# Optimization experiments

Hardware: AMD Instinct MI355X
Metric: run time of the kernel (lower is better)

Reference implementation:

```python
import jax, jax.numpy as jnp
import numpy as np

N_NODES = 50000
N_EDGES = 800000
IN_CH = 128
HEADS = 4
HID = 32  # per-head dim; heads*hid = 128
N_GRAPHS = 128


def setup_inputs() -> dict:
    key = jax.random.key(0)
    ks = jax.random.split(key, 32)
    d = {}
    d["x"] = jax.random.normal(ks[0], (N_NODES, IN_CH), dtype=jnp.float32)
    d["edge_index"] = jax.random.randint(ks[1], (2, N_EDGES), 0, N_NODES, dtype=jnp.int64)
    d["batch"] = jnp.sort(jax.random.randint(ks[2], (N_NODES,), 0, N_GRAPHS, dtype=jnp.int64))
    HD = HEADS * HID
    names = [("wq1", (IN_CH, HD)), ("bq1", (HD,)), ("wk1", (IN_CH, HD)), ("bk1", (HD,)),
             ("wv1", (IN_CH, HD)), ("bv1", (HD,)), ("ws1", (IN_CH, HD)), ("bs1", (HD,)),
             ("wq2", (HD, HD)), ("bq2", (HD,)), ("wk2", (HD, HD)), ("bk2", (HD,)),
             ("wv2", (HD, HD)), ("bv2", (HD,)), ("ws2", (HD, HD)), ("bs2", (HD,)),
             ("wl", (HD, HD)), ("bl", (HD,)), ("wl2", (HD, 1)), ("bl2", (1,))]
    for i, (nm, shp) in enumerate(names):
        d[nm] = jax.random.normal(ks[3 + i], shp, dtype=jnp.float32) * 0.05
    return d


def _transformer_conv(x, src, dst, wq, bq, wk, bk, wv, bv, ws, bs):
    """PyG TransformerConv: multi-head dot-product attention over edges,
    softmax normalized per destination node, plus linear root/skip term."""
    N = x.shape[0]
    q = (x @ wq + bq).reshape(N, HEADS, HID)
    k = (x @ wk + bk).reshape(N, HEADS, HID)
    v = (x @ wv + bv).reshape(N, HEADS, HID)
    # edge scores: [E, H]
    e = jnp.einsum('ehd,ehd->eh', q[dst], k[src]) * np.float32(1.0 / np.sqrt(HID))
    # segment softmax over incoming edges of each destination node
    m = jax.ops.segment_max(e, dst, num_segments=N)
    a = jnp.exp(e - m[dst])
    s = jax.ops.segment_sum(a, dst, num_segments=N)
    alpha = a / s[dst]  # [E, H]
    msg = alpha[:, :, None] * v[src]  # [E, H, D]
    out = jax.ops.segment_sum(msg, dst, num_segments=N).reshape(N, HEADS * HID)
    return out + x @ ws + bs  # root weight (skip) term


def reference(x, edge_index, batch,
              wq1, bq1, wk1, bk1, wv1, bv1, ws1, bs1,
              wq2, bq2, wk2, bk2, wv2, bv2, ws2, bs2,
              wl, bl, wl2, bl2):
    src, dst = edge_index[0], edge_index[1]
    h = _transformer_conv(x, src, dst, wq1, bq1, wk1, bk1, wv1, bv1, ws1, bs1)
    h = jax.nn.relu(h)
    h = _transformer_conv(h, src, dst, wq2, bq2, wk2, bk2, wv2, bv2, ws2, bs2)
    h = jax.nn.relu(h)
    h = h @ wl + bl
    h = h @ wl2 + bl2  # [N, 1]
    # global mean pool over graphs
    sums = jax.ops.segment_sum(h, batch, num_segments=N_GRAPHS)
    cnts = jax.ops.segment_sum(jnp.ones((h.shape[0], 1), h.dtype), batch, num_segments=N_GRAPHS)
    return sums / jnp.maximum(cnts, 1.0)
```

## Files before the change

### kernel.cpp

```cpp
#include <hip/hip_runtime.h>
#include <hip/hip_bf16.h>
#include <math.h>

#define NNODES 50000
#define NEDGES 800000
#define NGRAPHS 128
#define SCAN_B ((NNODES + 255) / 256)

typedef __attribute__((ext_vector_type(8))) short bf16x8;
typedef __attribute__((ext_vector_type(4))) float f32x4;

__device__ __forceinline__ unsigned short f2bf(float f) {
    unsigned int u = __float_as_uint(f);
    return (unsigned short)((u + 0x7FFFu + ((u >> 16) & 1u)) >> 16);
}
__device__ __forceinline__ float2 bf2f2(unsigned int u) {
    float2 f;
    f.x = __uint_as_float(u << 16);
    f.y = __uint_as_float(u & 0xFFFF0000u);
    return f;
}

__global__ void count_edges(const int* __restrict__ ei, int* __restrict__ cnt) {
    int e = blockIdx.x * 256 + threadIdx.x;
    if (e < NEDGES) atomicAdd(&cnt[ei[NEDGES + e]], 1);
}

__global__ __launch_bounds__(256)
void scan_pass1(const int* __restrict__ cnt, int* __restrict__ bsum) {
    const int t = threadIdx.x;
    const int i = blockIdx.x * 256 + t;
    int v = (i < NNODES) ? cnt[i] : 0;
#pragma unroll
    for (int off = 32; off > 0; off >>= 1) v += __shfl_xor(v, off, 64);
    __shared__ int ws[4];
    if ((t & 63) == 0) ws[t >> 6] = v;
    __syncthreads();
    if (t == 0) bsum[blockIdx.x] = ws[0] + ws[1] + ws[2] + ws[3];
}

__global__ __launch_bounds__(256)
void scan_pass2(const int* __restrict__ bsum, int* __restrict__ boff) {
    const int t = threadIdx.x;
    const int v = (t < SCAN_B) ? bsum[t] : 0;
    __shared__ int a[256];
    a[t] = v;
    __syncthreads();
    for (int off = 1; off < 256; off <<= 1) {
        const int u = (t >= off) ? a[t - off] : 0;
        __syncthreads();
        a[t] += u;
        __syncthreads();
    }
    if (t < SCAN_B) boff[t] = a[t] - v;
}

__global__ __launch_bounds__(256)
void scan_pass3(const int* __restrict__ cnt, const int* __restrict__ boff,
                int* __restrict__ rowptr, int* __restrict__ wpos) {
    const int t = threadIdx.x;
    const int i = blockIdx.x * 256 + t;
    const int v = (i < NNODES) ? cnt[i] : 0;
    __shared__ int a[256];
    a[t] = v;
    __syncthreads();
    for (int off = 1; off < 256; off <<= 1) {
        const int u = (t >= off) ? a[t - off] : 0;
        __syncthreads();
        a[t] += u;
        __syncthreads();
    }
    if (i < NNODES) {
        const int e = boff[blockIdx.x] + a[t] - v;
        rowptr[i] = e;
        wpos[i]   = e;
    }
    if (i == 0) rowptr[NNODES] = NEDGES;
}

__global__ void fill_csr(const int* __restrict__ ei, int* __restrict__ wpos,
                         int* __restrict__ colsrc) {
    int e = blockIdx.x * 256 + threadIdx.x;
    if (e < NEDGES) {
        int d = ei[NEDGES + e];
        int slot = atomicAdd(&wpos[d], 1);
        colsrc[slot] = ei[e];
    }
}

__global__ void fuse_wl(const float* __restrict__ wl, const float* __restrict__ bl,
                        const float* __restrict__ wl2, const float* __restrict__ bl2,
                        float* __restrict__ wf, float* __restrict__ bf) {
    int t = threadIdx.x;
    float s = 0.f;
    for (int j = 0; j < 128; ++j) s += wl[t * 128 + j] * wl2[j];
    wf[t] = s;
    if (t == 0) {
        float s2 = 0.f;
        for (int j = 0; j < 128; ++j) s2 += bl[j] * wl2[j];
        bf[0] = s2 + bl2[0];
    }
}

__global__ void prep_w(const float* __restrict__ wq, const float* __restrict__ wk,
                       const float* __restrict__ wv, const float* __restrict__ wsk,
                       unsigned short* __restrict__ Wt) {
    const int sel = blockIdx.y;
    const float* W = sel == 0 ? wq : sel == 1 ? wk : sel == 2 ? wv : wsk;
    const int idx = blockIdx.x * 256 + threadIdx.x;
    const int col = idx & 127;
    const int k   = idx >> 7;
    Wt[sel * 16384 + col * 128 + k] = f2bf(W[k * 128 + col]);
}

__global__ __launch_bounds__(256)
void gemm_qkvs(const float* __restrict__ F, const unsigned short* __restrict__ Wt,
               const float* __restrict__ bq, const float* __restrict__ bk,
               const float* __restrict__ bv, const float* __restrict__ bsk,
               float* __restrict__ Q, unsigned short* __restrict__ Kb,
               float* __restrict__ V, float* __restrict__ H) {
    __shared__ __align__(16) unsigned short As[128][136];
    __shared__ __align__(16) unsigned short Bt[64][136];
    const int t    = threadIdx.x;
    const int m0   = blockIdx.x * 128;
    const int lane = t & 63;
    const int w    = t >> 6;
    const int l15  = lane & 15;
    const int lg   = lane >> 4;

    {
        const int row = t >> 1;
        const int kh  = (t & 1) * 64;
        const int gr  = min(m0 + row, NNODES - 1);
        const float* src = &F[(size_t)gr * 128 + kh];
#pragma unroll
        for (int p = 0; p < 16; ++p) {
            const float4 v = *(const float4*)&src[p * 4];
            ushort4 u;
            u.x = f2bf(v.x); u.y = f2bf(v.y); u.z = f2bf(v.z); u.w = f2bf(v.w);
            *(ushort4*)&As[row][kh + p * 4] = u;
        }
    }

    for (int sl = 0; sl < 8; ++sl) {
        const int sel = sl >> 1;
        const int c0  = (sl & 1) * 64;
        const float* bias = sel == 0 ? bq : sel == 1 ? bk : sel == 2 ? bv : bsk;

        {
            const int col = t >> 2;
            const int kb  = (t & 3) * 32;
            const unsigned short* src = &Wt[sel * 16384 + (c0 + col) * 128 + kb];
#pragma unroll
            for (int p = 0; p < 4; ++p)
                *(uint4*)&Bt[col][kb + p * 8] = *(const uint4*)&src[p * 8];
        }
        __syncthreads();

        const float b0 = bias[c0 + l15];
        const float b1 = bias[c0 + 16 + l15];
        const float b2 = bias[c0 + 32 + l15];
        const float b3 = bias[c0 + 48 + l15];
        f32x4 a00 = {b0, b0, b0, b0}, a01 = {b1, b1, b1, b1},
              a02 = {b2, b2, b2, b2}, a03 = {b3, b3, b3, b3};
        f32x4 a10 = a00, a11 = a01, a12 = a02, a13 = a03;
#pragma unroll
        for (int ks = 0; ks < 4; ++ks) {
            const int kof = ks * 32 + lg * 8;
            const bf16x8 af0 = *(const bf16x8*)&As[w * 32 + l15][kof];
            const bf16x8 af1 = *(const bf16x8*)&As[w * 32 + 16 + l15][kof];
            const bf16x8 bf0 = *(const bf16x8*)&Bt[l15][kof];
            const bf16x8 bf1 = *(const bf16x8*)&Bt[16 + l15][kof];
            const bf16x8 bf2 = *(const bf16x8*)&Bt[32 + l15][kof];
            const bf16x8 bf3 = *(const bf16x8*)&Bt[48 + l15][kof];
            a00 = __builtin_amdgcn_mfma_f32_16x16x32_bf16(af0, bf0, a00, 0, 0, 0);
            a01 = __builtin_amdgcn_mfma_f32_16x16x32_bf16(af0, bf1, a01, 0, 0, 0);
            a02 = __builtin_amdgcn_mfma_f32_16x16x32_bf16(af0, bf2, a02, 0, 0, 0);
            a03 = __builtin_amdgcn_mfma_f32_16x16x32_bf16(af0, bf3, a03, 0, 0, 0);
            a10 = __builtin_amdgcn_mfma_f32_16x16x32_bf16(af1, bf0, a10, 0, 0, 0);
            a11 = __builtin_amdgcn_mfma_f32_16x16x32_bf16(af1, bf1, a11, 0, 0, 0);
            a12 = __builtin_amdgcn_mfma_f32_16x16x32_bf16(af1, bf2, a12, 0, 0, 0);
            a13 = __builtin_amdgcn_mfma_f32_16x16x32_bf16(af1, bf3, a13, 0, 0, 0);
        }
        __syncthreads();

        const int r0 = m0 + w * 32 + lg * 4;
        if (sel == 1) {
#define STB(ACC, RT, CT)                                                       \
            _Pragma("unroll")                                                  \
            for (int i = 0; i < 4; ++i) {                                      \
                const int gr = r0 + (RT) * 16 + i;                             \
                if (gr < NNODES)                                               \
                    Kb[(size_t)gr * 128 + c0 + (CT) * 16 + l15] = f2bf(ACC[i]);\
            }
            STB(a00, 0, 0) STB(a01, 0, 1) STB(a02, 0, 2) STB(a03, 0, 3)
            STB(a10, 1, 0) STB(a11, 1, 1) STB(a12, 1, 2) STB(a13, 1, 3)
#undef STB
        } else {
            float* O = sel == 0 ? Q : sel == 2 ? V : H;
#define ST(ACC, RT, CT)                                                        \
            _Pragma("unroll")                                                  \
            for (int i = 0; i < 4; ++i) {                                      \
                const int gr = r0 + (RT) * 16 + i;                             \
                if (gr < NNODES)                                               \
                    O[(size_t)gr * 128 + c0 + (CT) * 16 + l15] = ACC[i];       \
            }
            ST(a00, 0, 0) ST(a01, 0, 1) ST(a02, 0, 2) ST(a03, 0, 3)
            ST(a10, 1, 0) ST(a11, 1, 1) ST(a12, 1, 2) ST(a13, 1, 3)
#undef ST
        }
    }
}

template <bool FUSE_HEAD>
__global__ __launch_bounds__(128)
void attn_agg(const float* __restrict__ Q, const unsigned short* __restrict__ Kb,
              const float* __restrict__ V, float* __restrict__ H,
              const int* __restrict__ rowptr, const int* __restrict__ colsrc,
              const float* __restrict__ wf, float* __restrict__ r) {
    const int n = blockIdx.x * 2 + (threadIdx.x >> 6);
    const int l = threadIdx.x & 63;
    const int c = (l >> 4) * 32 + (l & 15) * 2;
    const float2 q2 = *(const float2*)&Q[(size_t)n * 128 + c];
    const float q0 = q2.x * 0.17677669529663687f;
    const float q1 = q2.y * 0.17677669529663687f;
    const int beg = rowptr[n], end = rowptr[n + 1];
    const int cnt = end - beg;

    float m = -INFINITY, s = 0.f, acc0 = 0.f, acc1 = 0.f;
    unsigned kuA = 0, kuB = 0;
    float vA0 = 0.f, vA1 = 0.f, vB0 = 0.f, vB1 = 0.f;
    if (cnt > 0) {
        const int s0 = colsrc[beg];
        kuA = *(const unsigned*)&Kb[(size_t)s0 * 128 + c];
        const float2 v = *(const float2*)&V[(size_t)s0 * 128 + c];
        vA0 = v.x; vA1 = v.y;
    }
    if (cnt > 1) {
        const int s1 = colsrc[beg + 1];
        kuB = *(const unsigned*)&Kb[(size_t)s1 * 128 + c];
        const float2 v = *(const float2*)&V[(size_t)s1 * 128 + c];
        vB0 = v.x; vB1 = v.y;
    }
    int i = beg;
    for (; i + 1 < end; i += 2) {
        const unsigned ka_u = kuA, kb_u = kuB;
        const float va0 = vA0, va1 = vA1, vb0 = vB0, vb1 = vB1;
        if (i + 2 < end) {
            const int s2 = colsrc[i + 2];
            kuA = *(const unsigned*)&Kb[(size_t)s2 * 128 + c];
            const float2 v = *(const float2*)&V[(size_t)s2 * 128 + c];
            vA0 = v.x; vA1 = v.y;
        }
        if (i + 3 < end) {
            const int s3 = colsrc[i + 3];
            kuB = *(const unsigned*)&Kb[(size_t)s3 * 128 + c];
            const float2 v = *(const float2*)&V[(size_t)s3 * 128 + c];
            vB0 = v.x; vB1 = v.y;
        }
        const float2 ka = bf2f2(ka_u), kb2 = bf2f2(kb_u);
        float p0 = fmaf(q0, ka.x, q1 * ka.y);
        float p1 = fmaf(q0, kb2.x, q1 * kb2.y);
#pragma unroll
        for (int off = 8; off > 0; off >>= 1) {
            p0 += __shfl_xor(p0, off, 16);
            p1 += __shfl_xor(p1, off, 16);
        }
        const float nm = fmaxf(fmaxf(p0, p1), m);
        const float sc = __expf(m - nm);
        const float w0 = __expf(p0 - nm);
        const float w1 = __expf(p1 - nm);
        s    = fmaf(s, sc, w0 + w1);
        acc0 = fmaf(acc0, sc, fmaf(w0, va0, w1 * vb0));
        acc1 = fmaf(acc1, sc, fmaf(w0, va1, w1 * vb1));
        m = nm;
    }
    if (i < end) {
        const float2 ka = bf2f2(kuA);
        float p0 = fmaf(q0, ka.x, q1 * ka.y);
#pragma unroll
        for (int off = 8; off > 0; off >>= 1) p0 += __shfl_xor(p0, off, 16);
        const float nm = fmaxf(p0, m);
        const float sc = __expf(m - nm);
        const float w0 = __expf(p0 - nm);
        s    = fmaf(s, sc, w0);
        acc0 = fmaf(acc0, sc, w0 * vA0);
        acc1 = fmaf(acc1, sc, w0 * vA1);
    }
    const float2 hv = *(const float2*)&H[(size_t)n * 128 + c];
    float o0 = hv.x, o1 = hv.y;
    if (cnt > 0) {
        const float inv = 1.f / s;
        o0 += acc0 * inv;
        o1 += acc1 * inv;
    }
    o0 = fmaxf(o0, 0.f);
    o1 = fmaxf(o1, 0.f);
    if (!FUSE_HEAD) {
        float2 o; o.x = o0; o.y = o1;
        *(float2*)&H[(size_t)n * 128 + c] = o;
    } else {
        float val = fmaf(o0, wf[c], o1 * wf[c + 1]);
#pragma unroll
        for (int off = 32; off > 0; off >>= 1) val += __shfl_xor(val, off, 64);
        if (l == 0) r[n] = val;
    }
}

__global__ __launch_bounds__(256)
void graph_pool(const float* __restrict__ r, const int* __restrict__ batch,
                const float* __restrict__ bf, float* __restrict__ out) {
    const int g = blockIdx.x;
    const int t = threadIdx.x;
    int lo = 0, hi = NNODES;
    while (lo < hi) { int mid = (lo + hi) >> 1; if (batch[mid] < g) lo = mid + 1; else hi = mid; }
    const int beg = lo;
    lo = beg; hi = NNODES;
    while (lo < hi) { int mid = (lo + hi) >> 1; if (batch[mid] < g + 1) lo = mid + 1; else hi = mid; }
    const int end = lo;

    float s = 0.f;
    for (int i = beg + t; i < end; i += 256) s += r[i];
#pragma unroll
    for (int off = 32; off > 0; off >>= 1) s += __shfl_xor(s, off, 64);
    __shared__ float pw[4];
    if ((t & 63) == 0) pw[t >> 6] = s;
    __syncthreads();
    if (t == 0) {
        const float cnt = (float)(end - beg);
        const float tot = pw[0] + pw[1] + pw[2] + pw[3] + cnt * bf[0];
        out[g] = tot / fmaxf(cnt, 1.f);
    }
}

extern "C" void kernel_launch(void* const* d_in, const int* in_sizes, int n_in,
                              void* d_out, int out_size, void* d_ws, size_t ws_size,
                              hipStream_t stream) {
    const float* x     = (const float*)d_in[0];
    const int*   ei    = (const int*)d_in[1];
    const int*   batch = (const int*)d_in[2];
    const float* wq1 = (const float*)d_in[3];  const float* bq1 = (const float*)d_in[4];
    const float* wk1 = (const float*)d_in[5];  const float* bk1 = (const float*)d_in[6];
    const float* wv1 = (const float*)d_in[7];  const float* bv1 = (const float*)d_in[8];
    const float* ws1 = (const float*)d_in[9];  const float* bs1 = (const float*)d_in[10];
    const float* wq2 = (const float*)d_in[11]; const float* bq2 = (const float*)d_in[12];
    const float* wk2 = (const float*)d_in[13]; const float* bk2 = (const float*)d_in[14];
    const float* wv2 = (const float*)d_in[15]; const float* bv2 = (const float*)d_in[16];
    const float* ws2 = (const float*)d_in[17]; const float* bs2 = (const float*)d_in[18];
    const float* wl  = (const float*)d_in[19]; const float* bl  = (const float*)d_in[20];
    const float* wl2 = (const float*)d_in[21]; const float* bl2 = (const float*)d_in[22];

    char* wsb = (char*)d_ws;
    size_t off = 0;
    auto carve = [&](size_t bytes) -> void* {
        void* p = wsb + off;
        off = (off + bytes + 255) & ~(size_t)255;
        return p;
    };
    const size_t NM = (size_t)NNODES * 128 * sizeof(float);
    float* Q      = (float*)carve(NM);
    unsigned short* Kb = (unsigned short*)carve((size_t)NNODES * 128 * 2);
    float* V      = (float*)carve(NM);
    float* H1     = (float*)carve(NM);
    float* H2     = (float*)carve(NM);
    int*   rowptr = (int*)carve((NNODES + 1) * sizeof(int));
    int*   wpos   = (int*)carve(NNODES * sizeof(int));
    int*   cnt    = (int*)carve(NNODES * sizeof(int));
    int*   colsrc = (int*)carve(NEDGES * sizeof(int));
    int*   bsum   = (int*)carve(256 * sizeof(int));
    int*   boff   = (int*)carve(256 * sizeof(int));
    float* wf     = (float*)carve(129 * sizeof(float));
    float* bf     = wf + 128;
    float* nodeval = (float*)carve(NNODES * sizeof(float));
    unsigned short* Wt1 = (unsigned short*)carve(65536 * sizeof(unsigned short));
    unsigned short* Wt2 = (unsigned short*)carve(65536 * sizeof(unsigned short));

    hipMemsetAsync(cnt, 0, NNODES * sizeof(int), stream);

    count_edges<<<(NEDGES + 255) / 256, 256, 0, stream>>>(ei, cnt);
    scan_pass1<<<SCAN_B, 256, 0, stream>>>(cnt, bsum);
    scan_pass2<<<1, 256, 0, stream>>>(bsum, boff);
    scan_pass3<<<SCAN_B, 256, 0, stream>>>(cnt, boff, rowptr, wpos);
    fill_csr<<<(NEDGES + 255) / 256, 256, 0, stream>>>(ei, wpos, colsrc);
    fuse_wl<<<1, 128, 0, stream>>>(wl, bl, wl2, bl2, wf, bf);
    prep_w<<<dim3(64, 4), 256, 0, stream>>>(wq1, wk1, wv1, ws1, Wt1);
    prep_w<<<dim3(64, 4), 256, 0, stream>>>(wq2, wk2, wv2, ws2, Wt2);

    const int ggrid = (NNODES + 127) / 128;
    const int agrid = NNODES / 2;
    gemm_qkvs<<<ggrid, 256, 0, stream>>>(x, Wt1, bq1, bk1, bv1, bs1, Q, Kb, V, H1);
    attn_agg<false><<<agrid, 128, 0, stream>>>(Q, Kb, V, H1, rowptr, colsrc,
                                               nullptr, nullptr);
    gemm_qkvs<<<ggrid, 256, 0, stream>>>(H1, Wt2, bq2, bk2, bv2, bs2, Q, Kb, V, H2);
    attn_agg<true><<<agrid, 128, 0, stream>>>(Q, Kb, V, H2, rowptr, colsrc,
                                              wf, nodeval);
    graph_pool<<<NGRAPHS, 256, 0, stream>>>(nodeval, batch, bf, (float*)d_out);
}
```

Before: 457.6 us.

## Store V in bf16 and process two edges per wavefront half in attention

The V projection is now written as bf16 instead of fp32, halving the bytes gathered per edge in the attention aggregation. The attention kernel is restructured so each half-wavefront handles a different edge, with each lane covering four channels instead of two. The two halves' online-softmax states are merged with cross-half shuffles at the end. This cuts gather traffic and shuffle depth per edge, but V now carries bf16 rounding error and each node's odd edge leaves one half idle.

Result: faster. 401.6 us (-12.2%).

```diff
diff --git a/kernel.cpp b/kernel.cpp
--- a/kernel.cpp
+++ b/kernel.cpp
@@ -118,7 +118,7 @@
                const float* __restrict__ bq, const float* __restrict__ bk,
                const float* __restrict__ bv, const float* __restrict__ bsk,
                float* __restrict__ Q, unsigned short* __restrict__ Kb,
-               float* __restrict__ V, float* __restrict__ H) {
+               unsigned short* __restrict__ Vb, float* __restrict__ H) {
     __shared__ __align__(16) unsigned short As[128][136];
     __shared__ __align__(16) unsigned short Bt[64][136];
     const int t    = threadIdx.x;
@@ -185,19 +185,20 @@
         __syncthreads();
 
         const int r0 = m0 + w * 32 + lg * 4;
-        if (sel == 1) {
+        if (sel == 1 || sel == 2) {
+            unsigned short* Ob = sel == 1 ? Kb : Vb;
 #define STB(ACC, RT, CT)                                                       \
             _Pragma("unroll")                                                  \
             for (int i = 0; i < 4; ++i) {                                      \
                 const int gr = r0 + (RT) * 16 + i;                             \
                 if (gr < NNODES)                                               \
-                    Kb[(size_t)gr * 128 + c0 + (CT) * 16 + l15] = f2bf(ACC[i]);\
+                    Ob[(size_t)gr * 128 + c0 + (CT) * 16 + l15] = f2bf(ACC[i]);\
             }
             STB(a00, 0, 0) STB(a01, 0, 1) STB(a02, 0, 2) STB(a03, 0, 3)
             STB(a10, 1, 0) STB(a11, 1, 1) STB(a12, 1, 2) STB(a13, 1, 3)
 #undef STB
         } else {
-            float* O = sel == 0 ? Q : sel == 2 ? V : H;
+            float* O = sel == 0 ? Q : H;
 #define ST(ACC, RT, CT)                                                        \
             _Pragma("unroll")                                                  \
             for (int i = 0; i < 4; ++i) {                                      \
@@ -215,94 +216,84 @@
 template <bool FUSE_HEAD>
 __global__ __launch_bounds__(128)
 void attn_agg(const float* __restrict__ Q, const unsigned short* __restrict__ Kb,
-              const float* __restrict__ V, float* __restrict__ H,
+              const unsigned short* __restrict__ Vb, float* __restrict__ H,
               const int* __restrict__ rowptr, const int* __restrict__ colsrc,
               const float* __restrict__ wf, float* __restrict__ r) {
-    const int n = blockIdx.x * 2 + (threadIdx.x >> 6);
-    const int l = threadIdx.x & 63;
-    const int c = (l >> 4) * 32 + (l & 15) * 2;
-    const float2 q2 = *(const float2*)&Q[(size_t)n * 128 + c];
-    const float q0 = q2.x * 0.17677669529663687f;
-    const float q1 = q2.y * 0.17677669529663687f;
+    const int n    = blockIdx.x * 2 + (threadIdx.x >> 6);
+    const int l    = threadIdx.x & 63;
+    const int half = l >> 5;
+    const int c    = (l & 31) * 4;
+    const float4 q4 = *(const float4*)&Q[(size_t)n * 128 + c];
+    const float sc_ = 0.17677669529663687f;
+    const float q0 = q4.x * sc_, q1 = q4.y * sc_, q2 = q4.z * sc_, q3 = q4.w * sc_;
     const int beg = rowptr[n], end = rowptr[n + 1];
     const int cnt = end - beg;
 
-    float m = -INFINITY, s = 0.f, acc0 = 0.f, acc1 = 0.f;
-    unsigned kuA = 0, kuB = 0;
-    float vA0 = 0.f, vA1 = 0.f, vB0 = 0.f, vB1 = 0.f;
+    float m = -INFINITY, s = 0.f;
+    float a0 = 0.f, a1 = 0.f, a2 = 0.f, a3 = 0.f;
+
+    uint2 ku, vu;
     if (cnt > 0) {
-        const int s0 = colsrc[beg];
-        kuA = *(const unsigned*)&Kb[(size_t)s0 * 128 + c];
-        const float2 v = *(const float2*)&V[(size_t)s0 * 128 + c];
-        vA0 = v.x; vA1 = v.y;
-    }
-    if (cnt > 1) {
-        const int s1 = colsrc[beg + 1];
-        kuB = *(const unsigned*)&Kb[(size_t)s1 * 128 + c];
-        const float2 v = *(const float2*)&V[(size_t)s1 * 128 + c];
-        vB0 = v.x; vB1 = v.y;
-    }
-    int i = beg;
-    for (; i + 1 < end; i += 2) {
-        const unsigned ka_u = kuA, kb_u = kuB;
-        const float va0 = vA0, va1 = vA1, vb0 = vB0, vb1 = vB1;
+        const int src = colsrc[min(beg + half, end - 1)];
+        ku = *(const uint2*)&Kb[(size_t)src * 128 + c];
+        vu = *(const uint2*)&Vb[(size_t)src * 128 + c];
+    }
+    for (int i = beg; i < end; i += 2) {
+        const uint2 kc = ku, vc = vu;
+        const bool valid = (i + half) < end;
         if (i + 2 < end) {
-            const int s2 = colsrc[i + 2];
-            kuA = *(const unsigned*)&Kb[(size_t)s2 * 128 + c];
-            const float2 v = *(const float2*)&V[(size_t)s2 * 128 + c];
-            vA0 = v.x; vA1 = v.y;
-        }
-        if (i + 3 < end) {
-            const int s3 = colsrc[i + 3];
-            kuB = *(const unsigned*)&Kb[(size_t)s3 * 128 + c];
-            const float2 v = *(const float2*)&V[(size_t)s3 * 128 + c];
-            vB0 = v.x; vB1 = v.y;
-        }
-        const float2 ka = bf2f2(ka_u), kb2 = bf2f2(kb_u);
-        float p0 = fmaf(q0, ka.x, q1 * ka.y);
-        float p1 = fmaf(q0, kb2.x, q1 * kb2.y);
-#pragma unroll
-        for (int off = 8; off > 0; off >>= 1) {
-            p0 += __shfl_xor(p0, off, 16);
-            p1 += __shfl_xor(p1, off, 16);
-        }
-        const float nm = fmaxf(fmaxf(p0, p1), m);
+            const int srcN = colsrc[min(i + 2 + half, end - 1)];
+            ku = *(const uint2*)&Kb[(size_t)srcN * 128 + c];
+            vu = *(const uint2*)&Vb[(size_t)srcN * 128 + c];
+        }
+        const float2 k01 = bf2f2(kc.x), k23 = bf2f2(kc.y);
+        float p = fmaf(q0, k01.x, fmaf(q1, k01.y, fmaf(q2, k23.x, q3 * k23.y)));
+        p += __shfl_xor(p, 4);
+        p += __shfl_xor(p, 2);
+        p += __shfl_xor(p, 1);
+        if (!valid) p = -INFINITY;
+        const float pO = __shfl_xor(p, 32);
+        const float nm = fmaxf(fmaxf(p, pO), m);
         const float sc = __expf(m - nm);
-        const float w0 = __expf(p0 - nm);
-        const float w1 = __expf(p1 - nm);
-        s    = fmaf(s, sc, w0 + w1);
-        acc0 = fmaf(acc0, sc, fmaf(w0, va0, w1 * vb0));
-        acc1 = fmaf(acc1, sc, fmaf(w0, va1, w1 * vb1));
+        const float w  = __expf(p - nm);
+        s = fmaf(s, sc, w);
+        const float2 v01 = bf2f2(vc.x), v23 = bf2f2(vc.y);
+        a0 = fmaf(a0, sc, w * v01.x);
+        a1 = fmaf(a1, sc, w * v01.y);
+        a2 = fmaf(a2, sc, w * v23.x);
+        a3 = fmaf(a3, sc, w * v23.y);
         m = nm;
     }
-    if (i < end) {
-        const float2 ka = bf2f2(kuA);
-        float p0 = fmaf(q0, ka.x, q1 * ka.y);
-#pragma unroll
-        for (int off = 8; off > 0; off >>= 1) p0 += __shfl_xor(p0, off, 16);
-        const float nm = fmaxf(p0, m);
-        const float sc = __expf(m - nm);
-        const float w0 = __expf(p0 - nm);
-        s    = fmaf(s, sc, w0);
-        acc0 = fmaf(acc0, sc, w0 * vA0);
-        acc1 = fmaf(acc1, sc, w0 * vA1);
-    }
-    const float2 hv = *(const float2*)&H[(size_t)n * 128 + c];
-    float o0 = hv.x, o1 = hv.y;
+    s  += __shfl_xor(s, 32);
+    a0 += __shfl_xor(a0, 32);
+    a1 += __shfl_xor(a1, 32);
+    a2 += __shfl_xor(a2, 32);
+    a3 += __shfl_xor(a3, 32);
+
+    const float4 hv = *(const float4*)&H[(size_t)n * 128 + c];
+    float o0 = hv.x, o1 = hv.y, o2 = hv.z, o3 = hv.w;
     if (cnt > 0) {
         const float inv = 1.f / s;
-        o0 += acc0 * inv;
-        o1 += acc1 * inv;
-    }
-    o0 = fmaxf(o0, 0.f);
-    o1 = fmaxf(o1, 0.f);
+        o0 = fmaf(a0, inv, o0);
+        o1 = fmaf(a1, inv, o1);
+        o2 = fmaf(a2, inv, o2);
+        o3 = fmaf(a3, inv, o3);
+    }
+    o0 = fmaxf(o0, 0.f); o1 = fmaxf(o1, 0.f);
+    o2 = fmaxf(o2, 0.f); o3 = fmaxf(o3, 0.f);
     if (!FUSE_HEAD) {
-        float2 o; o.x = o0; o.y = o1;
-        *(float2*)&H[(size_t)n * 128 + c] = o;
+        if (half == 0) {
+            float4 o; o.x = o0; o.y = o1; o.z = o2; o.w = o3;
+            *(float4*)&H[(size_t)n * 128 + c] = o;
+        }
     } else {
-        float val = fmaf(o0, wf[c], o1 * wf[c + 1]);
-#pragma unroll
-        for (int off = 32; off > 0; off >>= 1) val += __shfl_xor(val, off, 64);
+        float val = fmaf(o0, wf[c], fmaf(o1, wf[c + 1],
+                    fmaf(o2, wf[c + 2], o3 * wf[c + 3])));
+        val += __shfl_xor(val, 16);
+        val += __shfl_xor(val, 8);
+        val += __shfl_xor(val, 4);
+        val += __shfl_xor(val, 2);
+        val += __shfl_xor(val, 1);
         if (l == 0) r[n] = val;
     }
 }
@@ -360,7 +351,7 @@
     const size_t NM = (size_t)NNODES * 128 * sizeof(float);
     float* Q      = (float*)carve(NM);
     unsigned short* Kb = (unsigned short*)carve((size_t)NNODES * 128 * 2);
-    float* V      = (float*)carve(NM);
+    unsigned short* Vb = (unsigned short*)carve((size_t)NNODES * 128 * 2);
     float* H1     = (float*)carve(NM);
     float* H2     = (float*)carve(NM);
     int*   rowptr = (int*)carve((NNODES + 1) * sizeof(int));
@@ -388,11 +379,11 @@
 
     const int ggrid = (NNODES + 127) / 128;
     const int agrid = NNODES / 2;
-    gemm_qkvs<<<ggrid, 256, 0, stream>>>(x, Wt1, bq1, bk1, bv1, bs1, Q, Kb, V, H1);
-    attn_agg<false><<<agrid, 128, 0, stream>>>(Q, Kb, V, H1, rowptr, colsrc,
+    gemm_qkvs<<<ggrid, 256, 0, stream>>>(x, Wt1, bq1, bk1, bv1, bs1, Q, Kb, Vb, H1);
+    attn_agg<false><<<agrid, 128, 0, stream>>>(Q, Kb, Vb, H1, rowptr, colsrc,
                                                nullptr, nullptr);
-    gemm_qkvs<<<ggrid, 256, 0, stream>>>(H1, Wt2, bq2, bk2, bv2, bs2, Q, Kb, V, H2);
-    attn_agg<true><<<agrid, 128, 0, stream>>>(Q, Kb, V, H2, rowptr, colsrc,
+    gemm_qkvs<<<ggrid, 256, 0, stream>>>(H1, Wt2, bq2, bk2, bv2, bs2, Q, Kb, Vb, H2);
+    attn_agg<true><<<agrid, 128, 0, stream>>>(Q, Kb, Vb, H2, rowptr, colsrc,
                                               wf, nodeval);
     graph_pool<<<NGRAPHS, 256, 0, stream>>>(nodeval, batch, bf, (float*)d_out);
 }
```
